# Optimization experiments

Hardware: AMD Instinct MI355X
Metric: run time of the kernel (lower is better)

## Reference

```python
import jax, jax.numpy as jnp
import numpy as np

B = 64
FEATS = [96, 64, 64, 64]   # per-level input features
NCNT = [1, 8, 64, 512]     # per-level node counts
NODES = 512                # nodes at current depth (tree[-1])
DEG = 8                    # branching degree at this depth
IN_F = 64                  # features[depth]
OUT_F = 64                 # features[depth+1]
SUP = 640                  # in_f * 10 support hidden


def setup_inputs() -> dict:
    key = jax.random.key(0)
    ks = jax.random.split(key, 12)
    inp = {}
    for i in range(4):
        inp[f"x{i}"] = jax.random.normal(ks[i], (B, NCNT[i], FEATS[i]), jnp.float32)
        inp[f"W{i}"] = jax.random.normal(ks[4 + i], (FEATS[i], OUT_F), jnp.float32) / np.sqrt(FEATS[i]).astype(np.float32)
    inp["branch"] = jax.random.normal(ks[8], (NODES, IN_F, IN_F * DEG), jnp.float32) / np.float32(8.0)
    inp["Ws1"] = jax.random.normal(ks[9], (IN_F, SUP), jnp.float32) / np.float32(8.0)
    inp["Ws2"] = jax.random.normal(ks[10], (SUP, OUT_F), jnp.float32) / np.sqrt(SUP).astype(np.float32)
    bound = np.float32(1.0 / np.sqrt(OUT_F))
    inp["bias"] = jax.random.uniform(ks[11], (1, DEG, OUT_F), jnp.float32, -bound, bound)
    return inp


def _lrelu(v):
    return jnp.where(v > 0, v, 0.2 * v)


def reference(x0, x1, x2, x3, W0, W1, W2, W3, branch, Ws1, Ws2, bias):
    xs = [x0, x1, x2, x3]
    Ws = [W0, W1, W2, W3]
    # multi-depth linear sum: project each ancestor level, replicate each
    # node's vector contiguously down to `NODES` rows (torch repeat+view)
    y = jnp.zeros((B, NODES, OUT_F), jnp.float32)
    for x, W in zip(xs, Ws):
        t = x @ W                                   # (B, n_i, OUT_F)
        y = y + jnp.repeat(t, NODES // t.shape[1], axis=1)
    # branching: per-node weight slice (GEMV per node, shared over batch)
    xb = _lrelu(jnp.einsum('bnf,nfg->bng', x3, branch))  # (B, NODES, IN_F*DEG)
    xb = xb.reshape(B, NODES * DEG, IN_F)
    xb = (xb @ Ws1) @ Ws2                           # support MLP -> (B, NODES*DEG, OUT_F)
    y = xb + jnp.repeat(y, DEG, axis=1)             # y repeat(1,1,deg).view
    y = _lrelu(y + jnp.tile(bias, (1, NODES, 1)))   # bias.repeat(1, nodes, 1)
    return y
```

## Files before the change

### kernel.cpp

```cpp
#include <hip/hip_runtime.h>


typedef float f32x4 __attribute__((ext_vector_type(4)));
typedef __bf16 bf16x8 __attribute__((ext_vector_type(8)));

__device__ __forceinline__ unsigned short f2bf(float f) {
    union { float f; unsigned int u; } x; x.f = f;
    unsigned int r = x.u + 0x7FFFu + ((x.u >> 16) & 1u);
    return (unsigned short)(r >> 16);
}

#define LDP 72

__global__ __launch_bounds__(256) void tree_prep(
    const float* __restrict__ x0, const float* __restrict__ W0,
    const float* __restrict__ x1, const float* __restrict__ W1,
    const float* __restrict__ x2, const float* __restrict__ W2,
    const float* __restrict__ x3, const float* __restrict__ W3,
    const float* __restrict__ Ws1, const float* __restrict__ Ws2,
    float* __restrict__ ylg, unsigned short* __restrict__ xbf,
    unsigned short* __restrict__ wsF, unsigned short* __restrict__ w3f)
{
    const int t = threadIdx.x;
    const int blk = blockIdx.x;
    if (blk < 1024) {
        const int b = blk >> 4;
        const int g = ((blk & 15) << 2) + (t >> 6);
        const int f = t & 63;
        const float* xp = x0 + b * 96;
        float a0 = 0.f, a1 = 0.f;
        #pragma unroll 8
        for (int k = 0; k < 96; k += 2) {
            a0 += xp[k]     * W0[k * 64 + f];
            a1 += xp[k + 1] * W0[(k + 1) * 64 + f];
        }
        const float* x1p = x1 + b * 512 + (g >> 3) * 64;
        #pragma unroll 8
        for (int k = 0; k < 64; k += 2) {
            a0 += x1p[k]     * W1[k * 64 + f];
            a1 += x1p[k + 1] * W1[(k + 1) * 64 + f];
        }
        const float* x2p = x2 + b * 4096 + g * 64;
        #pragma unroll 8
        for (int k = 0; k < 64; k += 2) {
            a0 += x2p[k]     * W2[k * 64 + f];
            a1 += x2p[k + 1] * W2[(k + 1) * 64 + f];
        }
        const int mt = b >> 4, l4 = (b >> 2) & 3, r = b & 3;
        const int ft = f >> 4, l15 = f & 15;
        ylg[(size_t)((g * 4 + mt) * 4 + ft) * 256 + (l4 * 16 + l15) * 4 + r] = a0 + a1;
    } else if (blk < 3072) {
        const int bb = blk - 1024;
        const int b = bb >> 5, ngrp = bb & 31;
        const int n = ngrp * 16 + (t >> 4), k0 = 4 * (t & 15);
        float4 v = *(const float4*)(x3 + (size_t)b * 32768 + (size_t)n * 64 + k0);
        const int mt = b >> 4, l15b = b & 15, ks = k0 >> 5, l4k = (k0 >> 3) & 3, j = k0 & 7;
        union { unsigned short h[4]; uint2 u; } p;
        p.h[0] = f2bf(v.x); p.h[1] = f2bf(v.y); p.h[2] = f2bf(v.z); p.h[3] = f2bf(v.w);
        *(uint2*)&xbf[(size_t)n * 4096 + ((mt * 2 + ks) * 64 + l4k * 16 + l15b) * 8 + j] = p.u;
    } else if (blk < 3136) {
        __shared__ float red[4][64];
        const int c = blk - 3072;
        const int f = t & 63, q = t >> 6;
        const float* w1p = Ws1 + (size_t)c * 640 + q * 160;
        const float* w2p = Ws2 + (size_t)(q * 160) * 64 + f;
        float a0 = 0.f, a1 = 0.f;
        #pragma unroll 8
        for (int s = 0; s < 160; s += 2) {
            a0 += w1p[s]     * w2p[(size_t)s * 64];
            a1 += w1p[s + 1] * w2p[(size_t)(s + 1) * 64];
        }
        red[q][f] = a0 + a1;
        __syncthreads();
        if (q == 0) {
            const float v = red[0][f] + red[1][f] + red[2][f] + red[3][f];
            const int ks = c >> 5, l4c = (c >> 3) & 3, j = c & 7;
            wsF[((f >> 4) * 2 + ks) * 512 + (l4c * 16 + (f & 15)) * 8 + j] = f2bf(v);
        }
    } else {
        const int l = t & 63;
        #pragma unroll
        for (int it = 0; it < 2; ++it) {
            const int fh = it * 4 + (t >> 6);
            const int ft = fh >> 1, ks = fh & 1;
            const int f = ft * 16 + (l & 15);
            const int kb = ks * 32 + (l >> 4) * 8;
            union { unsigned short h[8]; uint4 u; } p;
            #pragma unroll
            for (int j = 0; j < 8; ++j) p.h[j] = f2bf(W3[(kb + j) * 64 + f]);
            *(uint4*)&w3f[((size_t)fh * 64 + l) * 8] = p.u;
        }
    }
}

__global__ __launch_bounds__(256, 3) void tree_main(
    const float* __restrict__ branch, const float* __restrict__ bias,
    const float* __restrict__ ylg, const unsigned short* __restrict__ xbf,
    const unsigned short* __restrict__ wsF, const unsigned short* __restrict__ w3f,
    float* __restrict__ out)
{
    __shared__ unsigned short Ts[4][64 * LDP];
    const int t = threadIdx.x;
    const int w = t >> 6, l = t & 63;
    const int l15 = l & 15, l4 = l >> 4;
    const int id = blockIdx.x * 4 + w;
    const int n = id >> 3, d = id & 7;
    const int g = n >> 3;
    unsigned short* ts = Ts[w];

    const float* brp = branch + (size_t)n * 32768 + d * 64;
    float raw[4][2][8];
    #pragma unroll
    for (int cP = 0; cP < 4; ++cP)
        #pragma unroll
        for (int ks = 0; ks < 2; ++ks)
            #pragma unroll
            for (int j = 0; j < 8; ++j)
                raw[cP][ks][j] = brp[(size_t)(32 * ks + 8 * l4 + j) * 512 + 16 * cP + l15];

    bf16x8 bx[4][2];
    #pragma unroll
    for (int bt = 0; bt < 4; ++bt)
        #pragma unroll
        for (int ks = 0; ks < 2; ++ks)
            bx[bt][ks] = *(const bf16x8*)(xbf + (size_t)n * 4096 +
                                          ((bt * 2 + ks) * 64 + l) * 8);

    #pragma unroll
    for (int cP = 0; cP < 4; ++cP) {
        bf16x8 pf0, pf1;
        {
            union { unsigned short h[8]; bf16x8 bv; } p0, p1;
            #pragma unroll
            for (int j = 0; j < 8; ++j) {
                p0.h[j] = f2bf(raw[cP][0][j]);
                p1.h[j] = f2bf(raw[cP][1][j]);
            }
            pf0 = p0.bv; pf1 = p1.bv;
        }
        #pragma unroll
        for (int bt = 0; bt < 4; ++bt) {
            f32x4 acc = {0.f, 0.f, 0.f, 0.f};
            acc = __builtin_amdgcn_mfma_f32_16x16x32_bf16(pf0, bx[bt][0], acc, 0, 0, 0);
            acc = __builtin_amdgcn_mfma_f32_16x16x32_bf16(pf1, bx[bt][1], acc, 0, 0, 0);
            union { unsigned short h[4]; uint2 u; } q;
            #pragma unroll
            for (int r = 0; r < 4; ++r) {
                float v = acc[r];
                v = fmaxf(v, 0.2f * v);
                q.h[r] = f2bf(v);
            }
            *(uint2*)&ts[(16 * bt + l15) * LDP + 16 * cP + 4 * l4] = q.u;
        }
    }

    bf16x8 w3[4][2], wf[4][2];
    #pragma unroll
    for (int ft = 0; ft < 4; ++ft)
        #pragma unroll
        for (int ks = 0; ks < 2; ++ks) {
            w3[ft][ks] = *(const bf16x8*)(w3f + (size_t)((ft * 2 + ks) * 64 + l) * 8);
            wf[ft][ks] = *(const bf16x8*)(wsF + (size_t)((ft * 2 + ks) * 64 + l) * 8);
        }
    float bv[4];
    #pragma unroll
    for (int ft = 0; ft < 4; ++ft) bv[ft] = bias[d * 64 + 16 * ft + l15];

    float* outp = out + (size_t)(n * 8 + d) * 64;
    #pragma unroll
    for (int bt = 0; bt < 4; ++bt) {
        f32x4 y[4];
        #pragma unroll
        for (int ft = 0; ft < 4; ++ft)
            y[ft] = *(const f32x4*)(ylg + (size_t)((g * 4 + bt) * 4 + ft) * 256 + l * 4);
        bf16x8 a20 = *(const bf16x8*)&ts[(16 * bt + l15) * LDP + 8 * l4];
        bf16x8 a21 = *(const bf16x8*)&ts[(16 * bt + l15) * LDP + 32 + 8 * l4];
        #pragma unroll
        for (int ft = 0; ft < 4; ++ft) {
            y[ft] = __builtin_amdgcn_mfma_f32_16x16x32_bf16(bx[bt][0], w3[ft][0], y[ft], 0, 0, 0);
            y[ft] = __builtin_amdgcn_mfma_f32_16x16x32_bf16(bx[bt][1], w3[ft][1], y[ft], 0, 0, 0);
            y[ft] = __builtin_amdgcn_mfma_f32_16x16x32_bf16(a20, wf[ft][0], y[ft], 0, 0, 0);
            y[ft] = __builtin_amdgcn_mfma_f32_16x16x32_bf16(a21, wf[ft][1], y[ft], 0, 0, 0);
        }
        #pragma unroll
        for (int ft = 0; ft < 4; ++ft)
            #pragma unroll
            for (int r = 0; r < 4; ++r) {
                float val = y[ft][r] + bv[ft];
                val = fmaxf(val, 0.2f * val);
                outp[(size_t)(16 * bt + 4 * l4 + r) * 262144 + 16 * ft + l15] = val;
            }
    }
}

extern "C" void kernel_launch(void* const* d_in, const int* in_sizes, int n_in,
                              void* d_out, int out_size, void* d_ws, size_t ws_size,
                              hipStream_t stream) {
    (void)in_sizes; (void)n_in; (void)out_size; (void)ws_size;
    const float* x0     = (const float*)d_in[0];
    const float* W0     = (const float*)d_in[1];
    const float* x1     = (const float*)d_in[2];
    const float* W1     = (const float*)d_in[3];
    const float* x2     = (const float*)d_in[4];
    const float* W2     = (const float*)d_in[5];
    const float* x3     = (const float*)d_in[6];
    const float* W3     = (const float*)d_in[7];
    const float* branch = (const float*)d_in[8];
    const float* Ws1    = (const float*)d_in[9];
    const float* Ws2    = (const float*)d_in[10];
    const float* bias   = (const float*)d_in[11];

    float* ylg          = (float*)d_ws;
    unsigned short* xbf = (unsigned short*)((char*)d_ws + 1048576);
    unsigned short* wsF = (unsigned short*)((char*)d_ws + 5242880);
    unsigned short* w3f = (unsigned short*)((char*)d_ws + 5251072);
    float* out = (float*)d_out;

    tree_prep<<<3137, 256, 0, stream>>>(x0, W0, x1, W1, x2, W2, x3, W3, Ws1, Ws2,
                                        ylg, xbf, wsF, w3f);
    tree_main<<<1024, 256, 0, stream>>>(branch, bias, ylg, xbf, wsF, w3f, out);
}
```

Baseline: 52.02 us.

## Stage outputs through LDS for coalesced float4 stores, regroup block per node-half

Each block now handles four consecutive degree slots of one node, so its outputs form contiguous 256-float rows per batch. Results go into a shared staging buffer and are written out as coalesced float4 stores instead of scattered scalar stores. The loop is reordered by batch tile, which shrinks the per-wave LDS tile and reloads weights inside the loop to cut live registers. This adds two block barriers per batch tile and more LDS traffic.

```diff
diff --git a/kernel.cpp b/kernel.cpp
--- a/kernel.cpp
+++ b/kernel.cpp
@@ -11,6 +11,7 @@
 }
 
 #define LDP 72
+#define SGP 260
 
 __global__ __launch_bounds__(256) void tree_prep(
     const float* __restrict__ x0, const float* __restrict__ W0,
@@ -99,14 +100,15 @@
     const unsigned short* __restrict__ wsF, const unsigned short* __restrict__ w3f,
     float* __restrict__ out)
 {
-    __shared__ unsigned short Ts[4][64 * LDP];
+    __shared__ float stage[16 * SGP];
+    __shared__ unsigned short tsb[4][16 * LDP];
     const int t = threadIdx.x;
     const int w = t >> 6, l = t & 63;
     const int l15 = l & 15, l4 = l >> 4;
-    const int id = blockIdx.x * 4 + w;
-    const int n = id >> 3, d = id & 7;
+    const int n = blockIdx.x >> 1, dh = blockIdx.x & 1;
+    const int d = dh * 4 + w;
     const int g = n >> 3;
-    unsigned short* ts = Ts[w];
+    unsigned short* ts = tsb[w];
 
     const float* brp = branch + (size_t)n * 32768 + d * 64;
     float raw[4][2][8];
@@ -126,23 +128,26 @@
             bx[bt][ks] = *(const bf16x8*)(xbf + (size_t)n * 4096 +
                                           ((bt * 2 + ks) * 64 + l) * 8);
 
+    bf16x8 pf[4][2];
     #pragma unroll
     for (int cP = 0; cP < 4; ++cP) {
-        bf16x8 pf0, pf1;
-        {
-            union { unsigned short h[8]; bf16x8 bv; } p0, p1;
-            #pragma unroll
-            for (int j = 0; j < 8; ++j) {
-                p0.h[j] = f2bf(raw[cP][0][j]);
-                p1.h[j] = f2bf(raw[cP][1][j]);
-            }
-            pf0 = p0.bv; pf1 = p1.bv;
-        }
-        #pragma unroll
-        for (int bt = 0; bt < 4; ++bt) {
+        union { unsigned short h[8]; bf16x8 bv; } p0, p1;
+        #pragma unroll
+        for (int j = 0; j < 8; ++j) {
+            p0.h[j] = f2bf(raw[cP][0][j]);
+            p1.h[j] = f2bf(raw[cP][1][j]);
+        }
+        pf[cP][0] = p0.bv; pf[cP][1] = p1.bv;
+    }
+
+    float* outb = out + (size_t)(8 * n + 4 * dh) * 64;
+    #pragma unroll
+    for (int bt = 0; bt < 4; ++bt) {
+        #pragma unroll
+        for (int cP = 0; cP < 4; ++cP) {
             f32x4 acc = {0.f, 0.f, 0.f, 0.f};
-            acc = __builtin_amdgcn_mfma_f32_16x16x32_bf16(pf0, bx[bt][0], acc, 0, 0, 0);
-            acc = __builtin_amdgcn_mfma_f32_16x16x32_bf16(pf1, bx[bt][1], acc, 0, 0, 0);
+            acc = __builtin_amdgcn_mfma_f32_16x16x32_bf16(pf[cP][0], bx[bt][0], acc, 0, 0, 0);
+            acc = __builtin_amdgcn_mfma_f32_16x16x32_bf16(pf[cP][1], bx[bt][1], acc, 0, 0, 0);
             union { unsigned short h[4]; uint2 u; } q;
             #pragma unroll
             for (int r = 0; r < 4; ++r) {
@@ -150,46 +155,37 @@
                 v = fmaxf(v, 0.2f * v);
                 q.h[r] = f2bf(v);
             }
-            *(uint2*)&ts[(16 * bt + l15) * LDP + 16 * cP + 4 * l4] = q.u;
-        }
-    }
-
-    bf16x8 w3[4][2], wf[4][2];
-    #pragma unroll
-    for (int ft = 0; ft < 4; ++ft)
-        #pragma unroll
-        for (int ks = 0; ks < 2; ++ks) {
-            w3[ft][ks] = *(const bf16x8*)(w3f + (size_t)((ft * 2 + ks) * 64 + l) * 8);
-            wf[ft][ks] = *(const bf16x8*)(wsF + (size_t)((ft * 2 + ks) * 64 + l) * 8);
-        }
-    float bv[4];
-    #pragma unroll
-    for (int ft = 0; ft < 4; ++ft) bv[ft] = bias[d * 64 + 16 * ft + l15];
-
-    float* outp = out + (size_t)(n * 8 + d) * 64;
-    #pragma unroll
-    for (int bt = 0; bt < 4; ++bt) {
-        f32x4 y[4];
-        #pragma unroll
-        for (int ft = 0; ft < 4; ++ft)
-            y[ft] = *(const f32x4*)(ylg + (size_t)((g * 4 + bt) * 4 + ft) * 256 + l * 4);
-        bf16x8 a20 = *(const bf16x8*)&ts[(16 * bt + l15) * LDP + 8 * l4];
-        bf16x8 a21 = *(const bf16x8*)&ts[(16 * bt + l15) * LDP + 32 + 8 * l4];
+            *(uint2*)&ts[l15 * LDP + 16 * cP + 4 * l4] = q.u;
+        }
+        bf16x8 a20 = *(const bf16x8*)&ts[l15 * LDP + 8 * l4];
+        bf16x8 a21 = *(const bf16x8*)&ts[l15 * LDP + 32 + 8 * l4];
         #pragma unroll
         for (int ft = 0; ft < 4; ++ft) {
-            y[ft] = __builtin_amdgcn_mfma_f32_16x16x32_bf16(bx[bt][0], w3[ft][0], y[ft], 0, 0, 0);
-            y[ft] = __builtin_amdgcn_mfma_f32_16x16x32_bf16(bx[bt][1], w3[ft][1], y[ft], 0, 0, 0);
-            y[ft] = __builtin_amdgcn_mfma_f32_16x16x32_bf16(a20, wf[ft][0], y[ft], 0, 0, 0);
-            y[ft] = __builtin_amdgcn_mfma_f32_16x16x32_bf16(a21, wf[ft][1], y[ft], 0, 0, 0);
-        }
-        #pragma unroll
-        for (int ft = 0; ft < 4; ++ft)
+            f32x4 y = *(const f32x4*)(ylg + (size_t)((g * 4 + bt) * 4 + ft) * 256 + l * 4);
+            bf16x8 w30 = *(const bf16x8*)(w3f + (size_t)((ft * 2 + 0) * 64 + l) * 8);
+            bf16x8 w31 = *(const bf16x8*)(w3f + (size_t)((ft * 2 + 1) * 64 + l) * 8);
+            bf16x8 wf0 = *(const bf16x8*)(wsF + (size_t)((ft * 2 + 0) * 64 + l) * 8);
+            bf16x8 wf1 = *(const bf16x8*)(wsF + (size_t)((ft * 2 + 1) * 64 + l) * 8);
+            y = __builtin_amdgcn_mfma_f32_16x16x32_bf16(bx[bt][0], w30, y, 0, 0, 0);
+            y = __builtin_amdgcn_mfma_f32_16x16x32_bf16(bx[bt][1], w31, y, 0, 0, 0);
+            y = __builtin_amdgcn_mfma_f32_16x16x32_bf16(a20, wf0, y, 0, 0, 0);
+            y = __builtin_amdgcn_mfma_f32_16x16x32_bf16(a21, wf1, y, 0, 0, 0);
+            const float bv = bias[d * 64 + 16 * ft + l15];
             #pragma unroll
             for (int r = 0; r < 4; ++r) {
-                float val = y[ft][r] + bv[ft];
+                float val = y[r] + bv;
                 val = fmaxf(val, 0.2f * val);
-                outp[(size_t)(16 * bt + 4 * l4 + r) * 262144 + 16 * ft + l15] = val;
+                stage[(4 * l4 + r) * SGP + w * 64 + 16 * ft + l15] = val;
             }
+        }
+        __syncthreads();
+        #pragma unroll
+        for (int i = 0; i < 4; ++i) {
+            const int bloc = 4 * i + w;
+            float4 v = *(const float4*)&stage[bloc * SGP + 4 * l];
+            *(float4*)(outb + (size_t)(16 * bt + bloc) * 262144 + 4 * l) = v;
+        }
+        __syncthreads();
     }
 }
 
```

After: 54.94 us. +5.6%, slower.
